# Optimization experiments

Measured on AMD Instinct MI355X. Metric: run time of the kernel, lower is better.

Reference implementation:

```python
import jax, jax.numpy as jnp
import numpy as np

B, S, D = 2, 2048, 1024
H = 16
HD = D // H  # 64


def _xavier(key, shape):
    fan_out, fan_in = shape
    limit = np.sqrt(6.0 / (fan_in + fan_out)).astype(np.float32)
    return jax.random.uniform(key, shape, jnp.float32, -limit, limit)


def setup_inputs() -> dict:
    key = jax.random.key(0)
    ks = jax.random.split(key, 6)
    return {
        "x": jax.random.normal(ks[0], (B, S, D), jnp.float32),
        "pos_bias": jax.random.normal(ks[1], (1, H, S, S), jnp.float32) * 0.02,
        "sinusoidal_pos": jax.random.normal(ks[2], (1, 1, S, HD), jnp.float32),
        "mask": jax.random.randint(ks[3], (1, 1, S, S), 0, 2, jnp.int32),
        "W_qkv": _xavier(ks[4], (3 * D, D)),
        "b_qkv": jnp.zeros((3 * D,), jnp.float32),
        "W_o": _xavier(ks[5], (D, D)),
        "b_o": jnp.zeros((D,), jnp.float32),
    }


def _rotate_half(t):
    # t: [..., HD]; reshape to [..., 2, HD//2], swap halves with sign flip
    t2 = t.reshape(*t.shape[:-1], 2, HD // 2)
    a, b = t2[..., 0, :], t2[..., 1, :]
    return jnp.concatenate((-b, a), axis=-1)


def _apply_rope(t, sinusoidal_pos):
    sp = sinusoidal_pos[:, :, -t.shape[-2]:]
    return t * jnp.cos(sp) + _rotate_half(t) * jnp.sin(sp)


def reference(x, pos_bias, sinusoidal_pos, mask, W_qkv, b_qkv, W_o, b_o):
    b, s, _ = x.shape
    qkv = x @ W_qkv.T + b_qkv                     # [B,S,3D]
    qkv = qkv.reshape(b, s, H, 3 * HD).transpose(0, 2, 1, 3)  # [B,H,S,3hd]
    q, k, v = jnp.split(qkv, 3, axis=-1)
    q = _apply_rope(q, sinusoidal_pos)
    k = _apply_rope(k, sinusoidal_pos)
    logits = jnp.einsum("bhqd,bhkd->bhqk", q, k)  # [B,H,S,S]
    logits = (logits + pos_bias) / np.sqrt(HD).astype(np.float32)
    logits = jnp.where(mask == 0, jnp.float32(-9e15), logits)
    attn = jax.nn.softmax(logits, axis=-1)
    vals = jnp.einsum("bhqk,bhkd->bhqd", attn, v)
    vals = vals.transpose(0, 2, 1, 3).reshape(b, s, D)
    return vals @ W_o.T + b_o
```

## Files before the change

### kernel.cpp

```cpp
#include <hip/hip_runtime.h>
#include <cmath>

#define B_ 2
#define S_ 2048
#define D_ 1024
#define H_ 16
#define HD_ 64

typedef __attribute__((ext_vector_type(8))) short bf16x8;
typedef __attribute__((ext_vector_type(4))) short bf16x4;
typedef __attribute__((ext_vector_type(4))) float floatx4;
#define MFMA_BF16(a, b, c) __builtin_amdgcn_mfma_f32_16x16x32_bf16(a, b, c, 0, 0, 0)

__device__ __forceinline__ ushort f2bf(float x) {
    union { float f; unsigned u; } v; v.f = x;
    unsigned u = v.u;
    return (ushort)((u + 0x7FFFu + ((u >> 16) & 1u)) >> 16);
}
__device__ __forceinline__ float bf2f(ushort b) {
    union { unsigned u; float f; } v; v.u = ((unsigned)b) << 16;
    return v.f;
}

__global__ __launch_bounds__(256) void f32_split_bf16(
    const float* __restrict__ in, ushort* __restrict__ hi,
    ushort* __restrict__ lo, int n4)
{
    int i = blockIdx.x * 256 + threadIdx.x;
    if (i >= n4) return;
    float4 v = ((const float4*)in)[i];
    bf16x4 h, l;
    float vv[4] = {v.x, v.y, v.z, v.w};
#pragma unroll
    for (int j = 0; j < 4; ++j) {
        ushort hb = f2bf(vv[j]);
        h[j] = (short)hb;
        l[j] = (short)f2bf(vv[j] - bf2f(hb));
    }
    ((bf16x4*)hi)[i] = h;
    ((bf16x4*)lo)[i] = l;
}

__global__ __launch_bounds__(256, 2) void gemm_mfma_split(
    const ushort* __restrict__ Ah, const ushort* __restrict__ Al,
    const ushort* __restrict__ Wh, const ushort* __restrict__ Wl,
    const float* __restrict__ bias, float* __restrict__ C,
    int M, int N, int K)
{
    constexpr int LD = 40;
    __shared__ ushort Ash[128][LD], Asl[128][LD], Wsh[128][LD], Wsl[128][LD];

    const int tid = threadIdx.x;
    const int lane = tid & 63;
    const int wv = tid >> 6;
    const int l15 = lane & 15;
    const int quad = lane >> 4;
    const int bm = blockIdx.y * 128;
    const int bn = blockIdx.x * 128;
    const int mw = (wv & 1) * 64;
    const int nw = (wv >> 1) * 64;

    floatx4 acc[4][4];
#pragma unroll
    for (int i = 0; i < 4; ++i)
#pragma unroll
        for (int j = 0; j < 4; ++j) acc[i][j] = (floatx4){0.f, 0.f, 0.f, 0.f};

    const int srow = tid >> 2;
    const int sc8 = (tid & 3) * 8;

    bf16x8 pAh[2], pAl[2], pWh[2], pWl[2];
    auto fetch = [&](int k0) {
#pragma unroll
        for (int u = 0; u < 2; ++u) {
            int r = srow + u * 64;
            pAh[u] = *(const bf16x8*)(Ah + (size_t)(bm + r) * K + k0 + sc8);
            pAl[u] = *(const bf16x8*)(Al + (size_t)(bm + r) * K + k0 + sc8);
            pWh[u] = *(const bf16x8*)(Wh + (size_t)(bn + r) * K + k0 + sc8);
            pWl[u] = *(const bf16x8*)(Wl + (size_t)(bn + r) * K + k0 + sc8);
        }
    };

    fetch(0);
    for (int k0 = 0; k0 < K; k0 += 32) {
        __syncthreads();
#pragma unroll
        for (int u = 0; u < 2; ++u) {
            int r = srow + u * 64;
            *(bf16x8*)&Ash[r][sc8] = pAh[u];
            *(bf16x8*)&Asl[r][sc8] = pAl[u];
            *(bf16x8*)&Wsh[r][sc8] = pWh[u];
            *(bf16x8*)&Wsl[r][sc8] = pWl[u];
        }
        __syncthreads();
        if (k0 + 32 < K) fetch(k0 + 32);

        bf16x8 aH[4], aL[4], bH[4], bL[4];
#pragma unroll
        for (int f = 0; f < 4; ++f) {
            aH[f] = *(const bf16x8*)&Ash[mw + f * 16 + l15][quad * 8];
            aL[f] = *(const bf16x8*)&Asl[mw + f * 16 + l15][quad * 8];
            bH[f] = *(const bf16x8*)&Wsh[nw + f * 16 + l15][quad * 8];
            bL[f] = *(const bf16x8*)&Wsl[nw + f * 16 + l15][quad * 8];
        }
#pragma unroll
        for (int mf = 0; mf < 4; ++mf)
#pragma unroll
            for (int nf = 0; nf < 4; ++nf) {
                acc[mf][nf] = MFMA_BF16(aH[mf], bH[nf], acc[mf][nf]);
                acc[mf][nf] = MFMA_BF16(aH[mf], bL[nf], acc[mf][nf]);
                acc[mf][nf] = MFMA_BF16(aL[mf], bH[nf], acc[mf][nf]);
            }
    }

#pragma unroll
    for (int mf = 0; mf < 4; ++mf)
#pragma unroll
        for (int nf = 0; nf < 4; ++nf) {
            int col = bn + nw + nf * 16 + l15;
            float bv = bias[col];
#pragma unroll
            for (int reg = 0; reg < 4; ++reg) {
                int row = bm + mw + mf * 16 + quad * 4 + reg;
                C[(size_t)row * N + col] = acc[mf][nf][reg] + bv;
            }
        }
}

__global__ __launch_bounds__(256) void rope_split_bf16(
    const float* __restrict__ qkv, const float* __restrict__ sp,
    ushort* __restrict__ q_hi, ushort* __restrict__ q_lo,
    ushort* __restrict__ k_hi, ushort* __restrict__ k_lo,
    ushort* __restrict__ v_t)
{
    __shared__ ushort VT[64][72];
    const int s0 = blockIdx.x * 64;
    const int h = blockIdx.y;
    const int b = blockIdx.z;
    const int d = threadIdx.x & 63;
    const int sw = threadIdx.x >> 6;
    const float sgn = (d < 32) ? -1.f : 1.f;

#pragma unroll 4
    for (int i = 0; i < 16; ++i) {
        int sl = i * 4 + sw;
        int s = s0 + sl;
        size_t base = ((size_t)(b * S_ + s)) * (3 * D_) + h * (3 * HD_) + d;
        float tq = qkv[base];
        float tk = qkv[base + HD_];
        float tv = qkv[base + 2 * HD_];
        float spv = sp[s * HD_ + d];
        float c = cosf(spv), sn = sinf(spv);
        float pq = __shfl_xor(tq, 32);
        float pk = __shfl_xor(tk, 32);
        float qv = (tq * c + sgn * pq * sn) * 0.125f;
        float kv = tk * c + sgn * pk * sn;

        size_t o = ((size_t)((b * H_ + h) * S_ + s)) * HD_ + d;
        ushort qh = f2bf(qv);
        q_hi[o] = qh; q_lo[o] = f2bf(qv - bf2f(qh));
        ushort kh = f2bf(kv);
        k_hi[o] = kh; k_lo[o] = f2bf(kv - bf2f(kh));
        VT[d][sl] = f2bf(tv);
    }
    __syncthreads();
    const int dd = threadIdx.x >> 2;
    const int c0 = (threadIdx.x & 3) * 16;
    size_t ob = ((size_t)((b * H_ + h) * HD_ + dd)) * S_ + s0 + c0;
    *(bf16x8*)(v_t + ob)     = *(const bf16x8*)&VT[dd][c0];
    *(bf16x8*)(v_t + ob + 8) = *(const bf16x8*)&VT[dd][c0 + 8];
}

__global__ __launch_bounds__(256, 3) void attn_flash_v3(
    const ushort* __restrict__ q_hi, const ushort* __restrict__ q_lo,
    const ushort* __restrict__ k_hi, const ushort* __restrict__ k_lo,
    const ushort* __restrict__ v_t, const float* __restrict__ pb,
    const int* __restrict__ mask,
    ushort* __restrict__ vals_hi, ushort* __restrict__ vals_lo)
{
    __shared__ ushort Kh[64][72];
    __shared__ ushort Kl[64][72];
    __shared__ ushort Vt[64][72];
    __shared__ ushort PBM[64][76];
    __shared__ ushort Ps[4][16][72];

    const int tid = threadIdx.x;
    const int lane = tid & 63;
    const int wv = tid >> 6;
    const int l15 = lane & 15;
    const int quad = lane >> 4;
    const int q0 = blockIdx.x * 64;
    const int h = blockIdx.y;
    const int b = blockIdx.z;
    const int qbase = q0 + wv * 16;

    const size_t bh_sd = ((size_t)(b * H_ + h)) * (size_t)S_ * HD_;

    const ushort* qrow_h = q_hi + bh_sd + (size_t)(qbase + l15) * HD_;
    const ushort* qrow_l = q_lo + bh_sd + (size_t)(qbase + l15) * HD_;
    bf16x8 qA_h0 = *(const bf16x8*)(qrow_h + quad * 8);
    bf16x8 qA_h1 = *(const bf16x8*)(qrow_h + 32 + quad * 8);
    bf16x8 qA_l0 = *(const bf16x8*)(qrow_l + quad * 8);
    bf16x8 qA_l1 = *(const bf16x8*)(qrow_l + 32 + quad * 8);

    floatx4 O4[4];
    float l_[4];
#pragma unroll
    for (int f = 0; f < 4; ++f) O4[f] = (floatx4){0.f, 0.f, 0.f, 0.f};
#pragma unroll
    for (int r = 0; r < 4; ++r) l_[r] = 0.f;

    const int kr = tid >> 3;
    const int kc8 = (tid & 7) * 8;
    const int pr = tid >> 4;
    const int pc4 = (tid & 15) * 4;

    bf16x8 pKh[2], pKl[2], pVt[2];
    float4 pPb[4];
    int4 pMk[4];
    auto fetch = [&](int kt) {
#pragma unroll
        for (int u = 0; u < 2; ++u) {
            int r = kr + u * 32;
            pKh[u] = *(const bf16x8*)(k_hi + bh_sd + (size_t)(kt + r) * HD_ + kc8);
            pKl[u] = *(const bf16x8*)(k_lo + bh_sd + (size_t)(kt + r) * HD_ + kc8);
            pVt[u] = *(const bf16x8*)(v_t + bh_sd + (size_t)r * S_ + kt + kc8);
        }
#pragma unroll
        for (int u = 0; u < 4; ++u) {
            int r = pr + u * 16;
            pPb[u] = *(const float4*)(pb + ((size_t)h * S_ + q0 + r) * S_ + kt + pc4);
            pMk[u] = *(const int4*)(mask + (size_t)(q0 + r) * S_ + kt + pc4);
        }
    };

    fetch(0);
    for (int kt = 0; kt < S_; kt += 64) {
        __syncthreads();
#pragma unroll
        for (int u = 0; u < 2; ++u) {
            int r = kr + u * 32;
            *(bf16x8*)&Kh[r][kc8] = pKh[u];
            *(bf16x8*)&Kl[r][kc8] = pKl[u];
            *(bf16x8*)&Vt[r][kc8] = pVt[u];
        }
#pragma unroll
        for (int u = 0; u < 4; ++u) {
            int r = pr + u * 16;
            bf16x4 w;
            w[0] = (short)f2bf(pMk[u].x == 0 ? -9e15f : pPb[u].x * 0.125f);
            w[1] = (short)f2bf(pMk[u].y == 0 ? -9e15f : pPb[u].y * 0.125f);
            w[2] = (short)f2bf(pMk[u].z == 0 ? -9e15f : pPb[u].z * 0.125f);
            w[3] = (short)f2bf(pMk[u].w == 0 ? -9e15f : pPb[u].w * 0.125f);
            *(bf16x4*)&PBM[r][pc4] = w;
        }
        __syncthreads();
        if (kt + 64 < S_) fetch(kt + 64);

        floatx4 S4[4];
#pragma unroll
        for (int nf = 0; nf < 4; ++nf) {
            const int krow = nf * 16 + l15;
            bf16x8 bh0 = *(const bf16x8*)&Kh[krow][quad * 8];
            bf16x8 bh1 = *(const bf16x8*)&Kh[krow][32 + quad * 8];
            bf16x8 bl0 = *(const bf16x8*)&Kl[krow][quad * 8];
            bf16x8 bl1 = *(const bf16x8*)&Kl[krow][32 + quad * 8];
            floatx4 a = (floatx4){0.f, 0.f, 0.f, 0.f};
            a = MFMA_BF16(qA_h0, bh0, a);
            a = MFMA_BF16(qA_h1, bh1, a);
            a = MFMA_BF16(qA_h0, bl0, a);
            a = MFMA_BF16(qA_h1, bl1, a);
            a = MFMA_BF16(qA_l0, bh0, a);
            a = MFMA_BF16(qA_l1, bh1, a);
            S4[nf] = a;
        }

#pragma unroll
        for (int nf = 0; nf < 4; ++nf) {
#pragma unroll
            for (int reg = 0; reg < 4; ++reg) {
                float x = S4[nf][reg] +
                    bf2f(PBM[wv * 16 + quad * 4 + reg][nf * 16 + l15]);
                float p = __expf(x);
                l_[reg] += p;
                Ps[wv][quad * 4 + reg][nf * 16 + l15] = f2bf(p);
            }
        }

        bf16x8 pA0 = *(const bf16x8*)&Ps[wv][l15][quad * 8];
        bf16x8 pA1 = *(const bf16x8*)&Ps[wv][l15][32 + quad * 8];
#pragma unroll
        for (int df = 0; df < 4; ++df) {
            const int vrow = df * 16 + l15;
            bf16x8 vB0 = *(const bf16x8*)&Vt[vrow][quad * 8];
            bf16x8 vB1 = *(const bf16x8*)&Vt[vrow][32 + quad * 8];
            O4[df] = MFMA_BF16(pA0, vB0, O4[df]);
            O4[df] = MFMA_BF16(pA1, vB1, O4[df]);
        }
    }

#pragma unroll
    for (int reg = 0; reg < 4; ++reg) {
        float lv = l_[reg];
        lv += __shfl_xor(lv, 1);
        lv += __shfl_xor(lv, 2);
        lv += __shfl_xor(lv, 4);
        lv += __shfl_xor(lv, 8);
        float inv = 1.f / lv;
        const int row = qbase + quad * 4 + reg;
        size_t ob = ((size_t)(b * S_ + row)) * D_ + h * HD_;
#pragma unroll
        for (int df = 0; df < 4; ++df) {
            float o = O4[df][reg] * inv;
            ushort hb = f2bf(o);
            vals_hi[ob + df * 16 + l15] = hb;
            vals_lo[ob + df * 16 + l15] = f2bf(o - bf2f(hb));
        }
    }
}

extern "C" void kernel_launch(void* const* d_in, const int* in_sizes, int n_in,
                              void* d_out, int out_size, void* d_ws, size_t ws_size,
                              hipStream_t stream) {
    const float* x      = (const float*)d_in[0];
    const float* pos_b  = (const float*)d_in[1];
    const float* sp     = (const float*)d_in[2];
    const int*   mask   = (const int*)d_in[3];
    const float* W_qkv  = (const float*)d_in[4];
    const float* b_qkv  = (const float*)d_in[5];
    const float* W_o    = (const float*)d_in[6];
    const float* b_o    = (const float*)d_in[7];
    float* out = (float*)d_out;

    char* w = (char*)d_ws;
    float*  qkv   = (float*)w;   w += (size_t)4096 * 3072 * 4;
    ushort* xv_hi = (ushort*)w;  w += (size_t)4096 * 1024 * 2;
    ushort* xv_lo = (ushort*)w;  w += (size_t)4096 * 1024 * 2;
    ushort* wq_hi = (ushort*)w;  w += (size_t)3072 * 1024 * 2;
    ushort* wq_lo = (ushort*)w;  w += (size_t)3072 * 1024 * 2;
    ushort* wo_hi = (ushort*)w;  w += (size_t)1024 * 1024 * 2;
    ushort* wo_lo = (ushort*)w;  w += (size_t)1024 * 1024 * 2;
    ushort* q_hi  = (ushort*)w;  w += (size_t)B_ * H_ * S_ * HD_ * 2;
    ushort* q_lo  = (ushort*)w;  w += (size_t)B_ * H_ * S_ * HD_ * 2;
    ushort* k_hi  = (ushort*)w;  w += (size_t)B_ * H_ * S_ * HD_ * 2;
    ushort* k_lo  = (ushort*)w;  w += (size_t)B_ * H_ * S_ * HD_ * 2;
    ushort* v_t   = (ushort*)w;  w += (size_t)B_ * H_ * S_ * HD_ * 2;

    f32_split_bf16<<<4096, 256, 0, stream>>>(x, xv_hi, xv_lo, 4096 * 1024 / 4);
    f32_split_bf16<<<3072, 256, 0, stream>>>(W_qkv, wq_hi, wq_lo, 3072 * 1024 / 4);
    f32_split_bf16<<<1024, 256, 0, stream>>>(W_o, wo_hi, wo_lo, 1024 * 1024 / 4);

    gemm_mfma_split<<<dim3(3072 / 128, 4096 / 128), 256, 0, stream>>>(
        xv_hi, xv_lo, wq_hi, wq_lo, b_qkv, qkv, 4096, 3072, 1024);

    rope_split_bf16<<<dim3(S_ / 64, H_, B_), 256, 0, stream>>>(
        qkv, sp, q_hi, q_lo, k_hi, k_lo, v_t);

    attn_flash_v3<<<dim3(S_ / 64, H_, B_), 256, 0, stream>>>(
        q_hi, q_lo, k_hi, k_lo, v_t, pos_b, mask, xv_hi, xv_lo);

    gemm_mfma_split<<<dim3(1024 / 128, 4096 / 128), 256, 0, stream>>>(
        xv_hi, xv_lo, wo_hi, wo_lo, b_o, out, 4096, 1024, 1024);
}
```

Before: 646.5 us.

## Process both batches per attention block to share pos_bias/mask loads, use exp2

```diff
diff --git a/kernel.cpp b/kernel.cpp
--- a/kernel.cpp
+++ b/kernel.cpp
@@ -12,6 +12,14 @@
 typedef __attribute__((ext_vector_type(4))) float floatx4;
 #define MFMA_BF16(a, b, c) __builtin_amdgcn_mfma_f32_16x16x32_bf16(a, b, c, 0, 0, 0)
 
+#define QSCL 0.18033688011112042f
+
+#if __has_builtin(__builtin_amdgcn_exp2f)
+#define EXP2F(x) __builtin_amdgcn_exp2f(x)
+#else
+#define EXP2F(x) __expf((x) * 0.6931471805599453f)
+#endif
+
 __device__ __forceinline__ ushort f2bf(float x) {
     union { float f; unsigned u; } v; v.f = x;
     unsigned u = v.u;
@@ -20,6 +28,11 @@
 __device__ __forceinline__ float bf2f(ushort b) {
     union { unsigned u; float f; } v; v.u = ((unsigned)b) << 16;
     return v.f;
+}
+__device__ __forceinline__ unsigned cvt_pk_bf16(float a, float b) {
+    unsigned r;
+    asm("v_cvt_pk_bf16_f32 %0, %1, %2" : "=v"(r) : "v"(a), "v"(b));
+    return r;
 }
 
 __global__ __launch_bounds__(256) void f32_split_bf16(
@@ -153,7 +166,7 @@
         float c = cosf(spv), sn = sinf(spv);
         float pq = __shfl_xor(tq, 32);
         float pk = __shfl_xor(tk, 32);
-        float qv = (tq * c + sgn * pq * sn) * 0.125f;
+        float qv = (tq * c + sgn * pq * sn) * QSCL;
         float kv = tk * c + sgn * pk * sn;
 
         size_t o = ((size_t)((b * H_ + h) * S_ + s)) * HD_ + d;
@@ -171,16 +184,16 @@
     *(bf16x8*)(v_t + ob + 8) = *(const bf16x8*)&VT[dd][c0 + 8];
 }
 
-__global__ __launch_bounds__(256, 3) void attn_flash_v3(
+__global__ __launch_bounds__(256, 2) void attn_flash_v4(
     const ushort* __restrict__ q_hi, const ushort* __restrict__ q_lo,
     const ushort* __restrict__ k_hi, const ushort* __restrict__ k_lo,
     const ushort* __restrict__ v_t, const float* __restrict__ pb,
     const int* __restrict__ mask,
     ushort* __restrict__ vals_hi, ushort* __restrict__ vals_lo)
 {
-    __shared__ ushort Kh[64][72];
-    __shared__ ushort Kl[64][72];
-    __shared__ ushort Vt[64][72];
+    __shared__ ushort Kh[2][64][72];
+    __shared__ ushort Kl[2][64][72];
+    __shared__ ushort Vt[2][64][72];
     __shared__ ushort PBM[64][76];
     __shared__ ushort Ps[4][16][72];
 
@@ -191,40 +204,46 @@
     const int quad = lane >> 4;
     const int q0 = blockIdx.x * 64;
     const int h = blockIdx.y;
-    const int b = blockIdx.z;
     const int qbase = q0 + wv * 16;
 
-    const size_t bh_sd = ((size_t)(b * H_ + h)) * (size_t)S_ * HD_;
-
-    const ushort* qrow_h = q_hi + bh_sd + (size_t)(qbase + l15) * HD_;
-    const ushort* qrow_l = q_lo + bh_sd + (size_t)(qbase + l15) * HD_;
-    bf16x8 qA_h0 = *(const bf16x8*)(qrow_h + quad * 8);
-    bf16x8 qA_h1 = *(const bf16x8*)(qrow_h + 32 + quad * 8);
-    bf16x8 qA_l0 = *(const bf16x8*)(qrow_l + quad * 8);
-    bf16x8 qA_l1 = *(const bf16x8*)(qrow_l + 32 + quad * 8);
-
-    floatx4 O4[4];
-    float l_[4];
-#pragma unroll
-    for (int f = 0; f < 4; ++f) O4[f] = (floatx4){0.f, 0.f, 0.f, 0.f};
-#pragma unroll
-    for (int r = 0; r < 4; ++r) l_[r] = 0.f;
+    bf16x8 qH0[2], qH1[2], qL0[2], qL1[2];
+#pragma unroll
+    for (int bb = 0; bb < 2; ++bb) {
+        const size_t bh = ((size_t)(bb * H_ + h)) * (size_t)S_ * HD_;
+        const ushort* qrh = q_hi + bh + (size_t)(qbase + l15) * HD_;
+        const ushort* qrl = q_lo + bh + (size_t)(qbase + l15) * HD_;
+        qH0[bb] = *(const bf16x8*)(qrh + quad * 8);
+        qH1[bb] = *(const bf16x8*)(qrh + 32 + quad * 8);
+        qL0[bb] = *(const bf16x8*)(qrl + quad * 8);
+        qL1[bb] = *(const bf16x8*)(qrl + 32 + quad * 8);
+    }
+
+    floatx4 O4[2][4];
+    float l_[2] = {0.f, 0.f};
+#pragma unroll
+    for (int bb = 0; bb < 2; ++bb)
+#pragma unroll
+        for (int f = 0; f < 4; ++f) O4[bb][f] = (floatx4){0.f, 0.f, 0.f, 0.f};
 
     const int kr = tid >> 3;
     const int kc8 = (tid & 7) * 8;
     const int pr = tid >> 4;
     const int pc4 = (tid & 15) * 4;
 
-    bf16x8 pKh[2], pKl[2], pVt[2];
+    bf16x8 pKh[2][2], pKl[2][2], pVt[2][2];
     float4 pPb[4];
     int4 pMk[4];
     auto fetch = [&](int kt) {
 #pragma unroll
-        for (int u = 0; u < 2; ++u) {
-            int r = kr + u * 32;
-            pKh[u] = *(const bf16x8*)(k_hi + bh_sd + (size_t)(kt + r) * HD_ + kc8);
-            pKl[u] = *(const bf16x8*)(k_lo + bh_sd + (size_t)(kt + r) * HD_ + kc8);
-            pVt[u] = *(const bf16x8*)(v_t + bh_sd + (size_t)r * S_ + kt + kc8);
+        for (int bb = 0; bb < 2; ++bb) {
+            const size_t bh = ((size_t)(bb * H_ + h)) * (size_t)S_ * HD_;
+#pragma unroll
+            for (int u = 0; u < 2; ++u) {
+                int r = kr + u * 32;
+                pKh[bb][u] = *(const bf16x8*)(k_hi + bh + (size_t)(kt + r) * HD_ + kc8);
+                pKl[bb][u] = *(const bf16x8*)(k_lo + bh + (size_t)(kt + r) * HD_ + kc8);
+                pVt[bb][u] = *(const bf16x8*)(v_t + bh + (size_t)r * S_ + kt + kc8);
+            }
         }
 #pragma unroll
         for (int u = 0; u < 4; ++u) {
@@ -238,83 +257,107 @@
     for (int kt = 0; kt < S_; kt += 64) {
         __syncthreads();
 #pragma unroll
-        for (int u = 0; u < 2; ++u) {
-            int r = kr + u * 32;
-            *(bf16x8*)&Kh[r][kc8] = pKh[u];
-            *(bf16x8*)&Kl[r][kc8] = pKl[u];
-            *(bf16x8*)&Vt[r][kc8] = pVt[u];
-        }
+        for (int bb = 0; bb < 2; ++bb)
+#pragma unroll
+            for (int u = 0; u < 2; ++u) {
+                int r = kr + u * 32;
+                *(bf16x8*)&Kh[bb][r][kc8] = pKh[bb][u];
+                *(bf16x8*)&Kl[bb][r][kc8] = pKl[bb][u];
+                *(bf16x8*)&Vt[bb][r][kc8] = pVt[bb][u];
+            }
 #pragma unroll
         for (int u = 0; u < 4; ++u) {
             int r = pr + u * 16;
-            bf16x4 w;
-            w[0] = (short)f2bf(pMk[u].x == 0 ? -9e15f : pPb[u].x * 0.125f);
-            w[1] = (short)f2bf(pMk[u].y == 0 ? -9e15f : pPb[u].y * 0.125f);
-            w[2] = (short)f2bf(pMk[u].z == 0 ? -9e15f : pPb[u].z * 0.125f);
-            w[3] = (short)f2bf(pMk[u].w == 0 ? -9e15f : pPb[u].w * 0.125f);
-            *(bf16x4*)&PBM[r][pc4] = w;
+            float w0 = pMk[u].x == 0 ? -3e30f : pPb[u].x * QSCL;
+            float w1 = pMk[u].y == 0 ? -3e30f : pPb[u].y * QSCL;
+            float w2 = pMk[u].z == 0 ? -3e30f : pPb[u].z * QSCL;
+            float w3 = pMk[u].w == 0 ? -3e30f : pPb[u].w * QSCL;
+            uint2 rr;
+            rr.x = cvt_pk_bf16(w0, w1);
+            rr.y = cvt_pk_bf16(w2, w3);
+            *(uint2*)&PBM[r][pc4] = rr;
         }
         __syncthreads();
         if (kt + 64 < S_) fetch(kt + 64);
 
-        floatx4 S4[4];
+        float pbv[4][4];
 #pragma unroll
         for (int nf = 0; nf < 4; ++nf) {
-            const int krow = nf * 16 + l15;
-            bf16x8 bh0 = *(const bf16x8*)&Kh[krow][quad * 8];
-            bf16x8 bh1 = *(const bf16x8*)&Kh[krow][32 + quad * 8];
-            bf16x8 bl0 = *(const bf16x8*)&Kl[krow][quad * 8];
-            bf16x8 bl1 = *(const bf16x8*)&Kl[krow][32 + quad * 8];
-            floatx4 a = (floatx4){0.f, 0.f, 0.f, 0.f};
-            a = MFMA_BF16(qA_h0, bh0, a);
-            a = MFMA_BF16(qA_h1, bh1, a);
-            a = MFMA_BF16(qA_h0, bl0, a);
-            a = MFMA_BF16(qA_h1, bl1, a);
-            a = MFMA_BF16(qA_l0, bh0, a);
-            a = MFMA_BF16(qA_l1, bh1, a);
-            S4[nf] = a;
-        }
-
-#pragma unroll
-        for (int nf = 0; nf < 4; ++nf) {
-#pragma unroll
-            for (int reg = 0; reg < 4; ++reg) {
-                float x = S4[nf][reg] +
-                    bf2f(PBM[wv * 16 + quad * 4 + reg][nf * 16 + l15]);
-                float p = __expf(x);
-                l_[reg] += p;
-                Ps[wv][quad * 4 + reg][nf * 16 + l15] = f2bf(p);
-            }
-        }
-
-        bf16x8 pA0 = *(const bf16x8*)&Ps[wv][l15][quad * 8];
-        bf16x8 pA1 = *(const bf16x8*)&Ps[wv][l15][32 + quad * 8];
-#pragma unroll
-        for (int df = 0; df < 4; ++df) {
-            const int vrow = df * 16 + l15;
-            bf16x8 vB0 = *(const bf16x8*)&Vt[vrow][quad * 8];
-            bf16x8 vB1 = *(const bf16x8*)&Vt[vrow][32 + quad * 8];
-            O4[df] = MFMA_BF16(pA0, vB0, O4[df]);
-            O4[df] = MFMA_BF16(pA1, vB1, O4[df]);
-        }
-    }
-
-#pragma unroll
-    for (int reg = 0; reg < 4; ++reg) {
-        float lv = l_[reg];
-        lv += __shfl_xor(lv, 1);
-        lv += __shfl_xor(lv, 2);
-        lv += __shfl_xor(lv, 4);
-        lv += __shfl_xor(lv, 8);
-        float inv = 1.f / lv;
-        const int row = qbase + quad * 4 + reg;
-        size_t ob = ((size_t)(b * S_ + row)) * D_ + h * HD_;
-#pragma unroll
-        for (int df = 0; df < 4; ++df) {
-            float o = O4[df][reg] * inv;
-            ushort hb = f2bf(o);
-            vals_hi[ob + df * 16 + l15] = hb;
-            vals_lo[ob + df * 16 + l15] = f2bf(o - bf2f(hb));
+            bf16x4 w = *(const bf16x4*)&PBM[wv * 16 + l15][nf * 16 + quad * 4];
+#pragma unroll
+            for (int reg = 0; reg < 4; ++reg) pbv[nf][reg] = bf2f((ushort)w[reg]);
+        }
+
+#pragma unroll
+        for (int bb = 0; bb < 2; ++bb) {
+            floatx4 S4[4];
+            __builtin_amdgcn_s_setprio(1);
+#pragma unroll
+            for (int nf = 0; nf < 4; ++nf) {
+                const int krow = nf * 16 + l15;
+                bf16x8 bh0 = *(const bf16x8*)&Kh[bb][krow][quad * 8];
+                bf16x8 bh1 = *(const bf16x8*)&Kh[bb][krow][32 + quad * 8];
+                bf16x8 bl0 = *(const bf16x8*)&Kl[bb][krow][quad * 8];
+                bf16x8 bl1 = *(const bf16x8*)&Kl[bb][krow][32 + quad * 8];
+                floatx4 a = (floatx4){0.f, 0.f, 0.f, 0.f};
+                a = MFMA_BF16(bh0, qH0[bb], a);
+                a = MFMA_BF16(bh1, qH1[bb], a);
+                a = MFMA_BF16(bl0, qH0[bb], a);
+                a = MFMA_BF16(bl1, qH1[bb], a);
+                a = MFMA_BF16(bh0, qL0[bb], a);
+                a = MFMA_BF16(bh1, qL1[bb], a);
+                S4[nf] = a;
+            }
+            __builtin_amdgcn_s_setprio(0);
+
+#pragma unroll
+            for (int nf = 0; nf < 4; ++nf) {
+                float p[4];
+#pragma unroll
+                for (int reg = 0; reg < 4; ++reg) {
+                    float x = S4[nf][reg] + pbv[nf][reg];
+                    p[reg] = EXP2F(x);
+                    l_[bb] += p[reg];
+                }
+                uint2 rr;
+                rr.x = cvt_pk_bf16(p[0], p[1]);
+                rr.y = cvt_pk_bf16(p[2], p[3]);
+                *(uint2*)&Ps[wv][l15][nf * 16 + quad * 4] = rr;
+            }
+
+            bf16x8 pA0 = *(const bf16x8*)&Ps[wv][l15][quad * 8];
+            bf16x8 pA1 = *(const bf16x8*)&Ps[wv][l15][32 + quad * 8];
+            __builtin_amdgcn_s_setprio(1);
+#pragma unroll
+            for (int df = 0; df < 4; ++df) {
+                const int vrow = df * 16 + l15;
+                bf16x8 vB0 = *(const bf16x8*)&Vt[bb][vrow][quad * 8];
+                bf16x8 vB1 = *(const bf16x8*)&Vt[bb][vrow][32 + quad * 8];
+                O4[bb][df] = MFMA_BF16(pA0, vB0, O4[bb][df]);
+                O4[bb][df] = MFMA_BF16(pA1, vB1, O4[bb][df]);
+            }
+            __builtin_amdgcn_s_setprio(0);
+        }
+    }
+
+#pragma unroll
+    for (int bb = 0; bb < 2; ++bb) {
+        float lv = l_[bb];
+        lv += __shfl_xor(lv, 16);
+        lv += __shfl_xor(lv, 32);
+        float linv = 1.f / lv;
+#pragma unroll
+        for (int reg = 0; reg < 4; ++reg) {
+            float inv = __shfl(linv, quad * 4 + reg);
+            const int row = qbase + quad * 4 + reg;
+            size_t ob = ((size_t)(bb * S_ + row)) * D_ + h * HD_;
+#pragma unroll
+            for (int df = 0; df < 4; ++df) {
+                float o = O4[bb][df][reg] * inv;
+                ushort hb = f2bf(o);
+                vals_hi[ob + df * 16 + l15] = hb;
+                vals_lo[ob + df * 16 + l15] = f2bf(o - bf2f(hb));
+            }
         }
     }
 }
@@ -356,7 +399,7 @@
     rope_split_bf16<<<dim3(S_ / 64, H_, B_), 256, 0, stream>>>(
         qkv, sp, q_hi, q_lo, k_hi, k_lo, v_t);
 
-    attn_flash_v3<<<dim3(S_ / 64, H_, B_), 256, 0, stream>>>(
+    attn_flash_v4<<<dim3(S_ / 64, H_), 256, 0, stream>>>(
         q_hi, q_lo, k_hi, k_lo, v_t, pos_b, mask, xv_hi, xv_lo);
 
     gemm_mfma_split<<<dim3(1024 / 128, 4096 / 128), 256, 0, stream>>>(
```

After: 629.8 us. -2.6%, faster.
